# Kernel optimization log

Hardware: AMD Instinct MI355X
Metric: run time of the kernel (lower is better)

## Reference

```python
import jax, jax.numpy as jnp
import numpy as np

SUBSTEP = 10
FRAMES = 24
T = FRAMES * SUBSTEP
DT = 1.0 / 60.0 / SUBSTEP
SLOPE_DEG = 20.0
COS_S = float(np.cos(np.deg2rad(SLOPE_DEG)))
SIN_S = float(np.sin(np.deg2rad(SLOPE_DEG)))
INIT_HEIGHT = 0.1
N_VERTS = 2_000_000
GRAVITY = jnp.array([0.0, -9.8, 0.0], dtype=jnp.float32)
CONTACT_N = jnp.array([-SIN_S, COS_S, 0.0], dtype=jnp.float32)
EPS = 1e-6


def quat_mul(a, b):
    w1, x1, y1, z1 = a[0], a[1], a[2], a[3]
    w2, x2, y2, z2 = b[0], b[1], b[2], b[3]
    return jnp.stack([
        w1 * w2 - x1 * x2 - y1 * y2 - z1 * z2,
        w1 * x2 + x1 * w2 + y1 * z2 - z1 * y2,
        w1 * y2 + y1 * w2 + z1 * x2 - x1 * z2,
        w1 * z2 + z1 * w2 + x1 * y2 - y1 * x2,
    ])


def quat_to_matrix(q):
    q = q / jnp.linalg.norm(q)
    w, x, y, z = q[0], q[1], q[2], q[3]
    return jnp.stack([
        jnp.stack([1 - 2 * y * y - 2 * z * z, 2 * x * y - 2 * w * z, 2 * x * z + 2 * w * y]),
        jnp.stack([2 * x * y + 2 * w * z, 1 - 2 * x * x - 2 * z * z, 2 * y * z - 2 * w * x]),
        jnp.stack([2 * x * z - 2 * w * y, 2 * y * z + 2 * w * x, 1 - 2 * x * x - 2 * y * y]),
    ])


def cross_matrix(a):
    z = jnp.zeros((), dtype=a.dtype)
    return jnp.stack([
        jnp.stack([z, -a[2], a[1]]),
        jnp.stack([a[2], z, -a[0]]),
        jnp.stack([-a[1], a[0], z]),
    ])


def setup_inputs() -> dict:
    key = jax.random.key(0)
    k1, k2, k3 = jax.random.split(key, 3)
    return {
        "x": jax.random.normal(k1, (N_VERTS, 3), dtype=jnp.float32) * 0.2,
        "mass_center": jnp.zeros((3,), dtype=jnp.float32),
        "init_trans": jax.random.normal(k2, (3,), dtype=jnp.float32) * 0.3 + jnp.array([0.3, 0.5, 0.0]),
        "init_quat": jnp.ones((4,), dtype=jnp.float32),
        "init_v": jax.random.normal(k3, (3,), dtype=jnp.float32) * 0.1,
        "kn": jnp.array([0.5], dtype=jnp.float32),
        "mu": jnp.array([0.4], dtype=jnp.float32),
        "linear_damping": jnp.array([0.999], dtype=jnp.float32),
        "angular_damping": jnp.array([0.998], dtype=jnp.float32),
    }


def _simulate(x, mass_center, init_trans, init_quat, init_v, kn, mu, linear_damping, angular_damping):
    n = x.shape[0]
    mass = jnp.asarray(float(n), dtype=x.dtype)  # unit mass per vertex
    inv_mass = 1.0 / mass
    r = x - mass_center
    # inertia_reference = sum_i m*( (r.r) I - outer(r,r) )
    inertia = jnp.sum(jnp.einsum('ni,ni->n', r, r)) * jnp.eye(3, dtype=x.dtype) - jnp.einsum('ni,nj->ij', r, r)
    kn0, mu0 = kn[0], mu[0]
    ld, ad = linear_damping[0], angular_damping[0]
    eye3 = jnp.eye(3, dtype=x.dtype)

    def step(carry, _):
        trans, quat, v, omega = carry
        Rm = quat_to_matrix(quat)
        Rx = x @ Rm.T                                   # [N,3]
        xi = trans + Rx + mass_center                   # world positions
        vi_all = v + jnp.cross(omega[None, :], Rx)      # per-vertex velocities
        d = xi @ CONTACT_N
        rel_v = vi_all @ CONTACT_N
        mask = (d < -COS_S * INIT_HEIGHT) & (rel_v < 0.0)
        num = jnp.sum(mask)
        numf = jnp.maximum(num, 1).astype(x.dtype)
        sum_pos = jnp.sum(x * mask[:, None].astype(x.dtype), axis=0)
        ri = sum_pos / numf
        Ri = Rm @ ri
        vi = v + jnp.cross(omega, Ri)
        v_n = jnp.dot(vi, CONTACT_N) * CONTACT_N
        v_t = vi - v_n
        vn_new = -kn0 * v_n
        alpha = jnp.maximum(1.0 - mu0 * (1.0 + kn0) * (jnp.linalg.norm(v_n) / (jnp.linalg.norm(v_t) + EPS)), 0.0)
        vi_new = vn_new + alpha * v_t
        I = Rm @ inertia @ Rm.T
        I_inv = jnp.linalg.inv(I)
        Rri = cross_matrix(Ri)
        kmat = inv_mass * eye3 - Rri @ I_inv @ Rri
        J = jnp.linalg.solve(kmat, vi_new - vi)
        hit = num > 0
        dv = jnp.where(hit, J * inv_mass, 0.0)
        domega = jnp.where(hit, I_inv @ Rri @ J, 0.0)
        v_new = (v + GRAVITY * DT) * ld + dv
        omega_new = omega * ad + domega
        trans_new = trans + DT * v_new
        wq = jnp.concatenate([jnp.zeros((1,), dtype=x.dtype), omega_new]) * (0.5 * DT)
        quat_new = quat + quat_mul(wq, quat)
        quat_new = quat_new / jnp.linalg.norm(quat_new)
        new_carry = (trans_new, quat_new, v_new, omega_new)
        return new_carry, jnp.concatenate([trans_new, quat_new])

    carry0 = (init_trans, init_quat / jnp.linalg.norm(init_quat), init_v, jnp.zeros(3, dtype=x.dtype))
    _, traj = jax.lax.scan(step, carry0, None, length=T)
    return traj  # [T, 7] = translation(3) + quaternion(4) per substep


def reference(x, mass_center, init_trans, init_quat, init_v, kn, mu, linear_damping, angular_damping):
    return _simulate(x, mass_center, init_trans, init_quat, init_v, kn, mu, linear_damping, angular_damping)
```

## Files before the change

kernel.cpp:

```cpp
#include <hip/hip_runtime.h>

#define GRID   256
#define BLOCK  512
#define NWAVES (BLOCK / 64)
#define CHUNK  7813
#define SLOTS  16
#define NREPT  64

typedef unsigned long long u64;

__device__ __forceinline__ u64 rec_load(const u64* p) {
  return __hip_atomic_load(p, __ATOMIC_RELAXED, __HIP_MEMORY_SCOPE_AGENT);
}
__device__ __forceinline__ void rec_store(u64* p, u64 v) {
  __hip_atomic_store(p, v, __ATOMIC_RELAXED, __HIP_MEMORY_SCOPE_AGENT);
}
__device__ __forceinline__ u64 rec_pack(float f, unsigned tag) {
  return (u64)__float_as_uint(f) | ((u64)tag << 32);
}

#define C_NX   ((float)(-0.3420201433256687))
#define C_NY   ((float)( 0.9396926207859084))
#define C_DTF  ((float)(1.0 / 60.0 / 10.0))
#define C_HDT  ((float)(0.5 * (1.0 / 60.0 / 10.0)))
#define C_DTH  ((float)(-0.9396926207859084 * 0.1))
#define C_GYDT (-9.8f * (float)(1.0 / 60.0 / 10.0))

__device__ __forceinline__ void mat3_mul(const float* A, const float* B, float* C) {
  #pragma unroll
  for (int i = 0; i < 3; ++i)
    #pragma unroll
    for (int j = 0; j < 3; ++j)
      C[i*3+j] = A[i*3+0]*B[0*3+j] + A[i*3+1]*B[1*3+j] + A[i*3+2]*B[2*3+j];
// ... 8 lines not shown
__device__ __forceinline__ void mat3_inv(const float* m, float* inv) {
  float A =  (m[4]*m[8] - m[5]*m[7]);
  float B = -(m[3]*m[8] - m[5]*m[6]);
  float C =  (m[3]*m[7] - m[4]*m[6]);
  float det = m[0]*A + m[1]*B + m[2]*C;
  float id = 1.0f / det;
  inv[0] = A * id;
  inv[1] = -(m[1]*m[8] - m[2]*m[7]) * id;
  inv[2] =  (m[1]*m[5] - m[2]*m[4]) * id;
  inv[3] = B * id;
  inv[4] =  (m[0]*m[8] - m[2]*m[6]) * id;
  inv[5] = -(m[0]*m[5] - m[2]*m[3]) * id;
  inv[6] = C * id;
  inv[7] = -(m[0]*m[7] - m[1]*m[6]) * id;
  inv[8] =  (m[0]*m[4] - m[1]*m[3]) * id;
}

__global__ __launch_bounds__(BLOCK, 2)
void sim_kernel(const float* __restrict__ xg,
                const float* __restrict__ mc_p,
                const float* __restrict__ itr_p,
                const float* __restrict__ iq_p,
                const float* __restrict__ iv_p,
                const float* __restrict__ kn_p,
                const float* __restrict__ mu_p,
                const float* __restrict__ ldp_p,
                const float* __restrict__ adp_p,
                float* __restrict__ out,
                u64* __restrict__ ws,
                int N, int T)
{
  const int tid  = threadIdx.x;
  const int bid  = blockIdx.x;
  const int lane = tid & 63;
  const int wid  = tid >> 6;

  __shared__ float s_redI[NWAVES * 6];
  __shared__ float s_red[2][NWAVES * 4];
  __shared__ float s_gat[NWAVES * 4];

  u64* part = ws;
  u64* tot  = ws + 2 * 4 * GRID;
  u64* bufI = ws + 2 * 4 * GRID + 2 * NREPT * 4;

  const float mc0 = mc_p[0], mc1 = mc_p[1], mc2 = mc_p[2];

  const int vstart = bid * CHUNK;
  int cl = N - vstart; if (cl > CHUNK) cl = CHUNK; if (cl < 0) cl = 0;

  const float NANF = __int_as_float(0x7fc00000);
  float xr0[SLOTS], xr1[SLOTS], xr2[SLOTS];
  #pragma unroll
  for (int s = 0; s < SLOTS; ++s) {
    const int i = tid + s * BLOCK;
    if (i < cl) {
      const float* p = xg + (size_t)(vstart + i) * 3;
      xr0[s] = p[0]; xr1[s] = p[1]; xr2[s] = p[2];
    } else {
      xr0[s] = NANF; xr1[s] = NANF; xr2[s] = NANF;
    }
  }

  {
    float v6[6] = {0,0,0,0,0,0};
    #pragma unroll
    for (int s = 0; s < SLOTS; ++s) {
      if (tid + s * BLOCK < cl) {
        float r0 = xr0[s] - mc0, r1 = xr1[s] - mc1, r2 = xr2[s] - mc2;
        v6[0] += r0*r0; v6[1] += r1*r1; v6[2] += r2*r2;
        v6[3] += r0*r1; v6[4] += r0*r2; v6[5] += r1*r2;
      }
    }
    #pragma unroll
    for (int off = 32; off > 0; off >>= 1)
      #pragma unroll
      for (int k = 0; k < 6; ++k) v6[k] += __shfl_down(v6[k], off, 64);
    if (lane == 0) {
      #pragma unroll
      for (int k = 0; k < 6; ++k) s_redI[wid * 6 + k] = v6[k];
    }
    __syncthreads();
    if (tid == 0) {
      float t6[6];
      #pragma unroll
      for (int k = 0; k < 6; ++k) {
        t6[k] = s_redI[k];
        #pragma unroll
        for (int w = 1; w < NWAVES; ++w) t6[k] += s_redI[w * 6 + k];
      }
      #pragma unroll
      for (int k = 0; k < 6; ++k) rec_store(bufI + k * GRID + bid, rec_pack(t6[k], 0xC0FFEEu));
    }
    __syncthreads();
  }

  float In[9];
  {
    float g6[6] = {0,0,0,0,0,0};
    if (tid < GRID) {
      u64 r[6];
      int f = 0;
      for (;;) {
        #pragma unroll
        for (int k = 0; k < 6; ++k) r[k] = rec_load(bufI + k * GRID + tid);
        bool ok = true;
        #pragma unroll
        for (int k = 0; k < 6; ++k) ok &= ((unsigned)(r[k] >> 32) == 0xC0FFEEu);
        if (ok) break;
        if ((++f & 15) == 0) __builtin_amdgcn_s_sleep(1);
      }
      #pragma unroll
      for (int k = 0; k < 6; ++k) g6[k] = __uint_as_float((unsigned)r[k]);
    }
    #pragma unroll
    for (int off = 32; off > 0; off >>= 1)
      #pragma unroll
      for (int k = 0; k < 6; ++k) g6[k] += __shfl_down(g6[k], off, 64);
    if (lane == 0) {
      #pragma unroll
      for (int k = 0; k < 6; ++k) s_redI[wid * 6 + k] = g6[k];
    }
    __syncthreads();
    float t6[6];
    #pragma unroll
    for (int k = 0; k < 6; ++k) {
      t6[k] = s_redI[k];
      #pragma unroll
      for (int w = 1; w < NWAVES; ++w) t6[k] += s_redI[w * 6 + k];
    }
    float trc = t6[0] + t6[1] + t6[2];
    In[0] = trc - t6[0]; In[4] = trc - t6[1]; In[8] = trc - t6[2];
    In[1] = -t6[3]; In[3] = -t6[3];
    In[2] = -t6[4]; In[6] = -t6[4];
    In[5] = -t6[5]; In[7] = -t6[5];
  }

  float tr0 = itr_p[0], tr1 = itr_p[1], tr2 = itr_p[2];
  float q0 = iq_p[0], q1 = iq_p[1], q2 = iq_p[2], q3 = iq_p[3];
  {
    float n0 = sqrtf(q0*q0 + q1*q1 + q2*q2 + q3*q3);
    q0 /= n0; q1 /= n0; q2 /= n0; q3 /= n0;
  }
  float v0 = iv_p[0], v1 = iv_p[1], v2 = iv_p[2];
  float om0 = 0.f, om1 = 0.f, om2 = 0.f;
  const float knv = kn_p[0], muv = mu_p[0], ldv = ldp_p[0], adv = adp_p[0];
  const float inv_mass = 1.0f / (float)N;

  float Rm[9], Ii[9];
  float pa0, pa1, pa2, pb0, pb1, pb2, pca, pcb;
  int skip;

  {
    float qn = sqrtf(q0*q0 + q1*q1 + q2*q2 + q3*q3);
    float w = q0/qn, xq = q1/qn, yq = q2/qn, zq = q3/qn;
    Rm[0] = 1.f - 2.f*yq*yq - 2.f*zq*zq; Rm[1] = 2.f*xq*yq - 2.f*w*zq; Rm[2] = 2.f*xq*zq + 2.f*w*yq;
    Rm[3] = 2.f*xq*yq + 2.f*w*zq; Rm[4] = 1.f - 2.f*xq*xq - 2.f*zq*zq; Rm[5] = 2.f*yq*zq - 2.f*w*xq;
    Rm[6] = 2.f*xq*zq - 2.f*w*yq; Rm[7] = 2.f*yq*zq + 2.f*w*xq; Rm[8] = 1.f - 2.f*xq*xq - 2.f*yq*yq;
    pa0 = Rm[0]*C_NX + Rm[3]*C_NY;
    pa1 = Rm[1]*C_NX + Rm[4]*C_NY;
    pa2 = Rm[2]*C_NX + Rm[5]*C_NY;
    float w0 = C_NY*om2, w1 = -C_NX*om2, w2 = C_NX*om1 - C_NY*om0;
    pb0 = Rm[0]*w0 + Rm[3]*w1 + Rm[6]*w2;
    pb1 = Rm[1]*w0 + Rm[4]*w1 + Rm[7]*w2;
    pb2 = Rm[2]*w0 + Rm[5]*w1 + Rm[8]*w2;
    pca = C_DTH - ((tr0 + mc0)*C_NX + (tr1 + mc1)*C_NY);
    pcb = -(v0*C_NX + v1*C_NY);
    skip = (om0 == 0.f && om1 == 0.f && om2 == 0.f && !(pcb > 0.f)) ? 1 : 0;
    float Tm[9]; mat3_mul(Rm, In, Tm);
    float Iw[9]; mat3_mul_bt(Tm, Rm, Iw);
    mat3_inv(Iw, Ii);
  }

  int pub = 0;
  for (int t = 0; t < T; ++t) {
    float tn = 0.f, tx = 0.f, ty = 0.f, tz = 0.f;

    if (!skip) {
      const int p = pub & 1;
      const unsigned want = (unsigned)(pub + 1);

      float acc0 = 0.f, acc1 = 0.f, acc2 = 0.f, acc3 = 0.f;
      #pragma unroll
      for (int s = 0; s < SLOTS; ++s) {
        const float x0 = xr0[s], x1 = xr1[s], x2 = xr2[s];
        const float da = x0*pa0 + x1*pa1 + x2*pa2;
        const float db = x0*pb0 + x1*pb1 + x2*pb2;
        if (da < pca && db < pcb) {
          acc0 += 1.f; acc1 += x0; acc2 += x1; acc3 += x2;
        }
      }
      #pragma unroll
      for (int off = 32; off > 0; off >>= 1) {
        acc0 += __shfl_down(acc0, off, 64);
        acc1 += __shfl_down(acc1, off, 64);
        acc2 += __shfl_down(acc2, off, 64);
        acc3 += __shfl_down(acc3, off, 64);
      }
      float* srA = s_red[p];
      if (lane == 0) {
        srA[wid*4+0] = acc0; srA[wid*4+1] = acc1;
        srA[wid*4+2] = acc2; srA[wid*4+3] = acc3;
      }
      __syncthreads();
      if (tid < 4) {
        float tw = srA[tid];
        #pragma unroll
        for (int w2 = 1; w2 < NWAVES; ++w2) tw += srA[w2*4 + tid];
        rec_store(part + (size_t)p * 4 * GRID + (size_t)tid * GRID + bid,
                  rec_pack(tw, want));
      }

      {
        float Tm[9]; mat3_mul(Rm, In, Tm);
        float Iw[9]; mat3_mul_bt(Tm, Rm, Iw);
        mat3_inv(Iw, Ii);
      }

      if (bid == 0) {
        float f0 = 0.f, f1 = 0.f, f2 = 0.f, f3 = 0.f;
        if (tid < GRID) {
          const u64* pp = part + (size_t)p * 4 * GRID + tid;
          u64 r0, r1, r2, r3;
          int fl = 0;
          for (;;) {
            r0 = rec_load(pp + 0 * GRID);
            r1 = rec_load(pp + 1 * GRID);
            r2 = rec_load(pp + 2 * GRID);
            r3 = rec_load(pp + 3 * GRID);
            if (((unsigned)(r0 >> 32) == want) && ((unsigned)(r1 >> 32) == want) &&
                ((unsigned)(r2 >> 32) == want) && ((unsigned)(r3 >> 32) == want)) break;
            if ((++fl & 15) == 0) __builtin_amdgcn_s_sleep(1);
          }
          f0 = __uint_as_float((unsigned)r0);
          f1 = __uint_as_float((unsigned)r1);
          f2 = __uint_as_float((unsigned)r2);
          f3 = __uint_as_float((unsigned)r3);
        }
        #pragma unroll
        for (int off = 32; off > 0; off >>= 1) {
          f0 += __shfl_down(f0, off, 64);
          f1 += __shfl_down(f1, off, 64);
          f2 += __shfl_down(f2, off, 64);
          f3 += __shfl_down(f3, off, 64);
        }
        if (lane == 0) {
          s_gat[wid*4+0] = f0; s_gat[wid*4+1] = f1;
          s_gat[wid*4+2] = f2; s_gat[wid*4+3] = f3;
        }
        __syncthreads();
        tn = s_gat[0]; tx = s_gat[1]; ty = s_gat[2]; tz = s_gat[3];
        #pragma unroll
        for (int w2 = 1; w2 < NWAVES; ++w2) {
          tn += s_gat[w2*4+0]; tx += s_gat[w2*4+1];
          ty += s_gat[w2*4+2]; tz += s_gat[w2*4+3];
        }
        if (tid < NREPT * 4) {
          const int w2 = tid & 3;
          const float val = (w2 == 0) ? tn : (w2 == 1) ? tx : (w2 == 2) ? ty : tz;
          rec_store(tot + (size_t)p * NREPT * 4 + tid, rec_pack(val, want));
        }
      } else {
        const u64* tp = tot + (size_t)p * NREPT * 4 + (size_t)(bid & (NREPT - 1)) * 4;
        u64 r0, r1, r2, r3;
        int fl = 0;
        for (;;) {
          r0 = rec_load(tp + 0); r1 = rec_load(tp + 1);
          r2 = rec_load(tp + 2); r3 = rec_load(tp + 3);
          if (((unsigned)(r0 >> 32) == want) && ((unsigned)(r1 >> 32) == want) &&
              ((unsigned)(r2 >> 32) == want) && ((unsigned)(r3 >> 32) == want)) break;
          if ((++fl & 31) == 0) __builtin_amdgcn_s_sleep(1);
        }
        tn = __uint_as_float((unsigned)r0);
        tx = __uint_as_float((unsigned)r1);
        ty = __uint_as_float((unsigned)r2);
        tz = __uint_as_float((unsigned)r3);
      }
      ++pub;
    }

    {
      float dv0 = 0.f, dv1 = 0.f, dv2 = 0.f, dm0 = 0.f, dm1 = 0.f, dm2 = 0.f;
      if (tn > 0.0f) {
        float numf = fmaxf(tn, 1.0f);
        float ri0 = tx/numf, ri1 = ty/numf, ri2 = tz/numf;
        float Ri0 = Rm[0]*ri0 + Rm[1]*ri1 + Rm[2]*ri2;
        float Ri1 = Rm[3]*ri0 + Rm[4]*ri1 + Rm[5]*ri2;
        float Ri2 = Rm[6]*ri0 + Rm[7]*ri1 + Rm[8]*ri2;
        float vi0 = v0 + om1*Ri2 - om2*Ri1;
        float vi1 = v1 + om2*Ri0 - om0*Ri2;
        float vi2 = v2 + om0*Ri1 - om1*Ri0;
        float vdn = vi0*C_NX + vi1*C_NY;
        float vn0 = vdn*C_NX, vn1 = vdn*C_NY;
        float vt0 = vi0 - vn0, vt1 = vi1 - vn1, vt2 = vi2;
        float nvn = sqrtf(vn0*vn0 + vn1*vn1);
        float nvt = sqrtf(vt0*vt0 + vt1*vt1 + vt2*vt2);
        float alpha = fmaxf(1.0f - muv*(1.0f + knv)*(nvn/(nvt + 1e-6f)), 0.0f);
        float dvi0 = (-knv*vn0 + alpha*vt0) - vi0;
        float dvi1 = (-knv*vn1 + alpha*vt1) - vi1;
        float dvi2 = (alpha*vt2) - vi2;
        float Cx[9] = {0.f, -Ri2, Ri1,  Ri2, 0.f, -Ri0,  -Ri1, Ri0, 0.f};
        float T2[9]; mat3_mul(Cx, Ii, T2);
        float T3[9]; mat3_mul(T2, Cx, T3);
        float Km[9];
        #pragma unroll
        for (int m = 0; m < 9; ++m) Km[m] = -T3[m];
        Km[0] += inv_mass; Km[4] += inv_mass; Km[8] += inv_mass;
        float Ki[9]; mat3_inv(Km, Ki);
        float J0 = Ki[0]*dvi0 + Ki[1]*dvi1 + Ki[2]*dvi2;
        float J1 = Ki[3]*dvi0 + Ki[4]*dvi1 + Ki[5]*dvi2;
        float J2 = Ki[6]*dvi0 + Ki[7]*dvi1 + Ki[8]*dvi2;
        dv0 = J0*inv_mass; dv1 = J1*inv_mass; dv2 = J2*inv_mass;
        float c0 = -Ri2*J1 + Ri1*J2;
        float c1 =  Ri2*J0 - Ri0*J2;
        float c2 = -Ri1*J0 + Ri0*J1;
        dm0 = Ii[0]*c0 + Ii[1]*c1 + Ii[2]*c2;
        dm1 = Ii[3]*c0 + Ii[4]*c1 + Ii[5]*c2;
        dm2 = Ii[6]*c0 + Ii[7]*c1 + Ii[8]*c2;
      }
      v0 = v0*ldv + dv0;
      v1 = (v1 + C_GYDT)*ldv + dv1;
      v2 = v2*ldv + dv2;
      om0 = om0*adv + dm0; om1 = om1*adv + dm1; om2 = om2*adv + dm2;
      tr0 += C_DTF*v0; tr1 += C_DTF*v1; tr2 += C_DTF*v2;
      float wx = om0*C_HDT, wy = om1*C_HDT, wz = om2*C_HDT;
      float dq0 = -wx*q1 - wy*q2 - wz*q3;
      float dq1 =  wx*q0 + wy*q3 - wz*q2;
      float dq2 =  wy*q0 + wz*q1 - wx*q3;
      float dq3 =  wz*q0 + wx*q2 - wy*q1;
      q0 += dq0; q1 += dq1; q2 += dq2; q3 += dq3;
      float qn2 = sqrtf(q0*q0 + q1*q1 + q2*q2 + q3*q3);
      q0 /= qn2; q1 /= qn2; q2 /= qn2; q3 /= qn2;
      if (bid == 0 && tid == 0) {
        float* o = out + (size_t)t * 7;
        o[0] = tr0; o[1] = tr1; o[2] = tr2;
        o[3] = q0;  o[4] = q1;  o[5] = q2;  o[6] = q3;
      }
      float qn = sqrtf(q0*q0 + q1*q1 + q2*q2 + q3*q3);
      float w = q0/qn, xq = q1/qn, yq = q2/qn, zq = q3/qn;
      Rm[0] = 1.f - 2.f*yq*yq - 2.f*zq*zq; Rm[1] = 2.f*xq*yq - 2.f*w*zq; Rm[2] = 2.f*xq*zq + 2.f*w*yq;
      Rm[3] = 2.f*xq*yq + 2.f*w*zq; Rm[4] = 1.f - 2.f*xq*xq - 2.f*zq*zq; Rm[5] = 2.f*yq*zq - 2.f*w*xq;
      Rm[6] = 2.f*xq*zq - 2.f*w*yq; Rm[7] = 2.f*yq*zq + 2.f*w*xq; Rm[8] = 1.f - 2.f*xq*xq - 2.f*yq*yq;
      pa0 = Rm[0]*C_NX + Rm[3]*C_NY;
      pa1 = Rm[1]*C_NX + Rm[4]*C_NY;
      pa2 = Rm[2]*C_NX + Rm[5]*C_NY;
      float w0 = C_NY*om2, w1 = -C_NX*om2, w2 = C_NX*om1 - C_NY*om0;
      pb0 = Rm[0]*w0 + Rm[3]*w1 + Rm[6]*w2;
      pb1 = Rm[1]*w0 + Rm[4]*w1 + Rm[7]*w2;
      pb2 = Rm[2]*w0 + Rm[5]*w1 + Rm[8]*w2;
      pca = C_DTH - ((tr0 + mc0)*C_NX + (tr1 + mc1)*C_NY);
      pcb = -(v0*C_NX + v1*C_NY);
      skip = (om0 == 0.f && om1 == 0.f && om2 == 0.f && !(pcb > 0.f)) ? 1 : 0;
    }
  }
}

extern "C" void kernel_launch(void* const* d_in, const int* in_sizes, int n_in,
                              void* d_out, int out_size, void* d_ws, size_t ws_size,
                              hipStream_t stream) {
  const float* x   = (const float*)d_in[0];
  const float* mc  = (const float*)d_in[1];
  const float* itr = (const float*)d_in[2];
  const float* iq  = (const float*)d_in[3];
  const float* iv  = (const float*)d_in[4];
  const float* kn  = (const float*)d_in[5];
  const float* mu  = (const float*)d_in[6];
  const float* ldp = (const float*)d_in[7];
  const float* adp = (const float*)d_in[8];
  float* out = (float*)d_out;
  u64* ws  = (u64*)d_ws;
  int N = in_sizes[0] / 3;
  int T = out_size / 7;

  void* args[] = {(void*)&x, (void*)&mc, (void*)&itr, (void*)&iq, (void*)&iv,
                  (void*)&kn, (void*)&mu, (void*)&ldp, (void*)&adp,
                  (void*)&out, (void*)&ws, (void*)&N, (void*)&T};
  hipLaunchCooperativeKernel((void*)sim_kernel, dim3(GRID), dim3(BLOCK),
                             args, 0, stream);
}
```

Baseline: 1.430 ms.

## Gather near-plane candidate vertices to leader block and iterate locally

Moves the per-step simulation onto block 0, which drives the other blocks through a request/mode protocol. Worker blocks scan their register-resident vertices against a widened plane threshold and publish the few near-contact candidates into a workspace buffer. The leader caches these candidates in LDS and runs several substeps on them alone, using a bound built from the maximum vertex radius to decide when to re-scan or fall back to a full grid reduction. This replaces the per-step grid-wide reduction and synchronisation with occasional scans, at the cost of a leader-serialised loop and correctness that depends on the conservative bound and the candidate capacity overflow path.

```diff
diff --git a/kernel.cpp b/kernel.cpp
--- a/kernel.cpp
+++ b/kernel.cpp
@@ -1,13 +1,23 @@
 #include <hip/hip_runtime.h>
 
-#define GRID   256
-#define BLOCK  512
-#define NWAVES (BLOCK / 64)
-#define CHUNK  7813
-#define SLOTS  16
-#define NREPT  64
+#define GRID    256
+#define BLOCK   512
+#define NWAVES  (BLOCK / 64)
+#define CHUNK   7813
+#define SLOTS   16
+#define NREPR   64
+#define CAP     96
+#define CSTRIDE 296
+#define CAPTOT  4096
+#define EPSB    0.03f
+
+#define MODE_SCAN 1u
+#define MODE_FULL 2u
+#define MODE_DONE 3u
 
 typedef unsigned long long u64;
+typedef unsigned int u32;
+
 
 __device__ __forceinline__ u64 rec_load(const u64* p) {
   return __hip_atomic_load(p, __ATOMIC_RELAXED, __HIP_MEMORY_SCOPE_AGENT);
@@ -17,6 +27,9 @@
 }
 __device__ __forceinline__ u64 rec_pack(float f, unsigned tag) {
   return (u64)__float_as_uint(f) | ((u64)tag << 32);
+}
+__device__ __forceinline__ u64 rec_pack_u(u32 v, unsigned tag) {
+  return (u64)v | ((u64)tag << 32);
 }
 
 #define C_NX   ((float)(-0.3420201433256687))
@@ -55,6 +68,167 @@
   inv[6] = C * id;
   inv[7] = -(m[0]*m[7] - m[1]*m[6]) * id;
   inv[8] =  (m[0]*m[4] - m[1]*m[3]) * id;
+}
+
+__device__ __forceinline__ void scan_publish(
+    const float* xr0, const float* xr1, const float* xr2,
+    float A0, float A1, float A2, float THR,
+    unsigned rrnd, u64* region, u32* s_wc )
+{
+  const int tid = threadIdx.x, lane = tid & 63, wid = tid >> 6;
+  #pragma unroll
+  for (int s = 0; s < SLOTS; ++s) {
+    float da = xr0[s]*A0 + xr1[s]*A1 + xr2[s]*A2;
+    u64 m = __ballot(da < THR);
+    if (lane == 0) s_wc[s*NWAVES + wid] = (u32)__popcll(m);
+  }
+  __syncthreads();
+  int runbase = 0;
+  #pragma unroll
+  for (int s = 0; s < SLOTS; ++s) {
+    int wb = 0, tot = 0;
+    #pragma unroll
+    for (int w = 0; w < NWAVES; ++w) {
+      u32 c = s_wc[s*NWAVES + w];
+      if (w < wid) wb += (int)c;
+      tot += (int)c;
+    }
+    const float x0 = xr0[s], x1 = xr1[s], x2 = xr2[s];
+    const float da = x0*A0 + x1*A1 + x2*A2;
+    const bool pred = (da < THR);
+    const u64 m = __ballot(pred);
+    if (pred) {
+      int pos = runbase + wb + (int)__popcll(m & ((1ull << lane) - 1ull));
+      if (pos < CAP) {
+        u64* dp = region + 1 + 3*(size_t)pos;
+        rec_store(dp + 0, rec_pack(x0, rrnd));
+        rec_store(dp + 1, rec_pack(x1, rrnd));
+        rec_store(dp + 2, rec_pack(x2, rrnd));
+      }
+    }
+    runbase += tot;
+  }
+  if (tid == 0) rec_store(region, rec_pack_u((u32)runbase, rrnd));
+  __syncthreads();
+}
+
+__device__ __forceinline__ void full_publish(
+    const float* xr0, const float* xr1, const float* xr2,
+    float A0, float A1, float A2, float CAv,
+    float B0, float B1, float B2, float CBv,
+    unsigned rrnd, u64* part, int bid, float* s_red)
+{
+  const int tid = threadIdx.x, lane = tid & 63, wid = tid >> 6;
+  float a0 = 0.f, a1 = 0.f, a2 = 0.f, a3 = 0.f;
+  #pragma unroll
+  for (int s = 0; s < SLOTS; ++s) {
+    const float x0 = xr0[s], x1 = xr1[s], x2 = xr2[s];
+    const float da = x0*A0 + x1*A1 + x2*A2;
+    const float db = x0*B0 + x1*B1 + x2*B2;
+    if (da < CAv && db < CBv) { a0 += 1.f; a1 += x0; a2 += x1; a3 += x2; }
+  }
+  #pragma unroll
+  for (int off = 32; off > 0; off >>= 1) {
+    a0 += __shfl_down(a0, off, 64);
+    a1 += __shfl_down(a1, off, 64);
+    a2 += __shfl_down(a2, off, 64);
+    a3 += __shfl_down(a3, off, 64);
+  }
+  if (lane == 0) {
+    s_red[wid*4+0] = a0; s_red[wid*4+1] = a1;
+    s_red[wid*4+2] = a2; s_red[wid*4+3] = a3;
+  }
+  __syncthreads();
+  if (tid < 4) {
+    float tw = s_red[tid];
+    #pragma unroll
+    for (int w = 1; w < NWAVES; ++w) tw += s_red[w*4 + tid];
+    rec_store(part + (size_t)tid * GRID + bid, rec_pack(tw, rrnd));
+  }
+  __syncthreads();
+}
+
+__device__ __forceinline__ void leader_step(
+    float tn, float tx, float ty, float tz,
+    float& tr0, float& tr1, float& tr2,
+    float& q0, float& q1, float& q2, float& q3,
+    float& v0, float& v1, float& v2,
+    float& om0, float& om1, float& om2,
+    float (&Rm)[9], const float (&In)[9],
+    float knv, float muv, float ldv, float adv, float inv_mass,
+    float mc0, float mc1,
+    float* s_plane, float* outp)
+{
+  float dv0 = 0.f, dv1 = 0.f, dv2 = 0.f, dm0 = 0.f, dm1 = 0.f, dm2 = 0.f;
+  if (tn > 0.0f) {
+    float Tm[9]; mat3_mul(Rm, In, Tm);
+    float Iw[9]; mat3_mul_bt(Tm, Rm, Iw);
+    float Ii[9]; mat3_inv(Iw, Ii);
+    float numf = fmaxf(tn, 1.0f);
+    float ri0 = tx/numf, ri1 = ty/numf, ri2 = tz/numf;
+    float Ri0 = Rm[0]*ri0 + Rm[1]*ri1 + Rm[2]*ri2;
+    float Ri1 = Rm[3]*ri0 + Rm[4]*ri1 + Rm[5]*ri2;
+    float Ri2 = Rm[6]*ri0 + Rm[7]*ri1 + Rm[8]*ri2;
+    float vi0 = v0 + om1*Ri2 - om2*Ri1;
+    float vi1 = v1 + om2*Ri0 - om0*Ri2;
+    float vi2 = v2 + om0*Ri1 - om1*Ri0;
+    float vdn = vi0*C_NX + vi1*C_NY;
+    float vn0 = vdn*C_NX, vn1 = vdn*C_NY;
+    float vt0 = vi0 - vn0, vt1 = vi1 - vn1, vt2 = vi2;
+    float nvn = sqrtf(vn0*vn0 + vn1*vn1);
+    float nvt = sqrtf(vt0*vt0 + vt1*vt1 + vt2*vt2);
+    float alpha = fmaxf(1.0f - muv*(1.0f + knv)*(nvn/(nvt + 1e-6f)), 0.0f);
+    float dvi0 = (-knv*vn0 + alpha*vt0) - vi0;
+    float dvi1 = (-knv*vn1 + alpha*vt1) - vi1;
+    float dvi2 = (alpha*vt2) - vi2;
+    float Cx[9] = {0.f, -Ri2, Ri1,  Ri2, 0.f, -Ri0,  -Ri1, Ri0, 0.f};
+    float T2[9]; mat3_mul(Cx, Ii, T2);
+    float T3[9]; mat3_mul(T2, Cx, T3);
+    float Km[9];
+    #pragma unroll
+    for (int m = 0; m < 9; ++m) Km[m] = -T3[m];
+    Km[0] += inv_mass; Km[4] += inv_mass; Km[8] += inv_mass;
+    float Ki[9]; mat3_inv(Km, Ki);
+    float J0 = Ki[0]*dvi0 + Ki[1]*dvi1 + Ki[2]*dvi2;
+    float J1 = Ki[3]*dvi0 + Ki[4]*dvi1 + Ki[5]*dvi2;
+    float J2 = Ki[6]*dvi0 + Ki[7]*dvi1 + Ki[8]*dvi2;
+    dv0 = J0*inv_mass; dv1 = J1*inv_mass; dv2 = J2*inv_mass;
+    float c0 = -Ri2*J1 + Ri1*J2;
+    float c1 =  Ri2*J0 - Ri0*J2;
+    float c2 = -Ri1*J0 + Ri0*J1;
+    dm0 = Ii[0]*c0 + Ii[1]*c1 + Ii[2]*c2;
+    dm1 = Ii[3]*c0 + Ii[4]*c1 + Ii[5]*c2;
+    dm2 = Ii[6]*c0 + Ii[7]*c1 + Ii[8]*c2;
+  }
+  v0 = v0*ldv + dv0;
+  v1 = (v1 + C_GYDT)*ldv + dv1;
+  v2 = v2*ldv + dv2;
+  om0 = om0*adv + dm0; om1 = om1*adv + dm1; om2 = om2*adv + dm2;
+  tr0 += C_DTF*v0; tr1 += C_DTF*v1; tr2 += C_DTF*v2;
+  float wx = om0*C_HDT, wy = om1*C_HDT, wz = om2*C_HDT;
+  float dq0 = -wx*q1 - wy*q2 - wz*q3;
+  float dq1 =  wx*q0 + wy*q3 - wz*q2;
+  float dq2 =  wy*q0 + wz*q1 - wx*q3;
+  float dq3 =  wz*q0 + wx*q2 - wy*q1;
+  q0 += dq0; q1 += dq1; q2 += dq2; q3 += dq3;
+  float qn2 = sqrtf(q0*q0 + q1*q1 + q2*q2 + q3*q3);
+  q0 /= qn2; q1 /= qn2; q2 /= qn2; q3 /= qn2;
+  outp[0] = tr0; outp[1] = tr1; outp[2] = tr2;
+  outp[3] = q0;  outp[4] = q1;  outp[5] = q2;  outp[6] = q3;
+  float qn = sqrtf(q0*q0 + q1*q1 + q2*q2 + q3*q3);
+  float w = q0/qn, xq = q1/qn, yq = q2/qn, zq = q3/qn;
+  Rm[0] = 1.f - 2.f*yq*yq - 2.f*zq*zq; Rm[1] = 2.f*xq*yq - 2.f*w*zq; Rm[2] = 2.f*xq*zq + 2.f*w*yq;
+  Rm[3] = 2.f*xq*yq + 2.f*w*zq; Rm[4] = 1.f - 2.f*xq*xq - 2.f*zq*zq; Rm[5] = 2.f*yq*zq - 2.f*w*xq;
+  Rm[6] = 2.f*xq*zq - 2.f*w*yq; Rm[7] = 2.f*yq*zq + 2.f*w*xq; Rm[8] = 1.f - 2.f*xq*xq - 2.f*yq*yq;
+  s_plane[0] = Rm[0]*C_NX + Rm[3]*C_NY;
+  s_plane[1] = Rm[1]*C_NX + Rm[4]*C_NY;
+  s_plane[2] = Rm[2]*C_NX + Rm[5]*C_NY;
+  float w0 = C_NY*om2, w1 = -C_NX*om2, w2 = C_NX*om1 - C_NY*om0;
+  s_plane[4] = Rm[0]*w0 + Rm[3]*w1 + Rm[6]*w2;
+  s_plane[5] = Rm[1]*w0 + Rm[4]*w1 + Rm[7]*w2;
+  s_plane[6] = Rm[2]*w0 + Rm[5]*w1 + Rm[8]*w2;
+  s_plane[3] = C_DTH - ((tr0 + mc0)*C_NX + (tr1 + mc1)*C_NY);
+  s_plane[7] = -(v0*C_NX + v1*C_NY);
 }
 
 __global__ __launch_bounds__(BLOCK, 2)
@@ -76,13 +250,25 @@
   const int lane = tid & 63;
   const int wid  = tid >> 6;
 
-  __shared__ float s_redI[NWAVES * 6];
-  __shared__ float s_red[2][NWAVES * 4];
-  __shared__ float s_gat[NWAVES * 4];
-
-  u64* part = ws;
-  u64* tot  = ws + 2 * 4 * GRID;
-  u64* bufI = ws + 2 * 4 * GRID + 2 * NREPT * 4;
+  __shared__ float s_redI[NWAVES * 7];
+  __shared__ float s_red[NWAVES * 4];
+  __shared__ float s_plane[8];
+  __shared__ u32   s_reqw[16];
+  __shared__ u32   s_cnt[GRID];
+  __shared__ u32   s_wc[SLOTS * NWAVES];
+  __shared__ u32   s_act;
+  __shared__ u32   s_total;
+
+  extern __shared__ float dyn[];
+  float* cx = dyn;
+  float* cy = dyn + CAPTOT;
+  float* cz = dyn + 2 * CAPTOT;
+  u32*   cmap = (u32*)(dyn + 3 * CAPTOT);
+
+  u64* req  = ws;
+  u64* part = ws + 1024;
+  u64* bufI = ws + 2048;
+  u64* cand = ws + 3840;
 
   const float mc0 = mc_p[0], mc1 = mc_p[1], mc2 = mc_p[2];
 
@@ -103,294 +289,344 @@
   }
 
   {
-    float v6[6] = {0,0,0,0,0,0};
+    float v7[7] = {0,0,0,0,0,0,0};
     #pragma unroll
     for (int s = 0; s < SLOTS; ++s) {
       if (tid + s * BLOCK < cl) {
         float r0 = xr0[s] - mc0, r1 = xr1[s] - mc1, r2 = xr2[s] - mc2;
-        v6[0] += r0*r0; v6[1] += r1*r1; v6[2] += r2*r2;
-        v6[3] += r0*r1; v6[4] += r0*r2; v6[5] += r1*r2;
-      }
-    }
-    #pragma unroll
-    for (int off = 32; off > 0; off >>= 1)
-      #pragma unroll
-      for (int k = 0; k < 6; ++k) v6[k] += __shfl_down(v6[k], off, 64);
+        v7[0] += r0*r0; v7[1] += r1*r1; v7[2] += r2*r2;
+        v7[3] += r0*r1; v7[4] += r0*r2; v7[5] += r1*r2;
+        float n2 = xr0[s]*xr0[s] + xr1[s]*xr1[s] + xr2[s]*xr2[s];
+        v7[6] = fmaxf(v7[6], n2);
+      }
+    }
+    #pragma unroll
+    for (int off = 32; off > 0; off >>= 1) {
+      #pragma unroll
+      for (int k = 0; k < 6; ++k) v7[k] += __shfl_down(v7[k], off, 64);
+      v7[6] = fmaxf(v7[6], __shfl_down(v7[6], off, 64));
+    }
     if (lane == 0) {
       #pragma unroll
-      for (int k = 0; k < 6; ++k) s_redI[wid * 6 + k] = v6[k];
+      for (int k = 0; k < 7; ++k) s_redI[wid * 7 + k] = v7[k];
     }
     __syncthreads();
     if (tid == 0) {
-      float t6[6];
-      #pragma unroll
-      for (int k = 0; k < 6; ++k) {
-        t6[k] = s_redI[k];
+      float t7[7];
+      #pragma unroll
+      for (int k = 0; k < 7; ++k) t7[k] = s_redI[k];
+      #pragma unroll
+      for (int w = 1; w < NWAVES; ++w) {
         #pragma unroll
-        for (int w = 1; w < NWAVES; ++w) t6[k] += s_redI[w * 6 + k];
-      }
-      #pragma unroll
-      for (int k = 0; k < 6; ++k) rec_store(bufI + k * GRID + bid, rec_pack(t6[k], 0xC0FFEEu));
+        for (int k = 0; k < 6; ++k) t7[k] += s_redI[w * 7 + k];
+        t7[6] = fmaxf(t7[6], s_redI[w * 7 + 6]);
+      }
+      #pragma unroll
+      for (int k = 0; k < 7; ++k)
+        rec_store(bufI + (size_t)k * GRID + bid, rec_pack(t7[k], 0xC0FFEEu));
     }
     __syncthreads();
   }
 
+  if (bid != 0) {
+    unsigned rrnd = 1;
+    for (;;) {
+      if (tid < 16) {
+        const u64* rl = req + (size_t)(bid & (NREPR - 1)) * 16 + tid;
+        u64 r; int f = 0;
+        for (;;) {
+          r = rec_load(rl);
+          if ((unsigned)(r >> 32) == rrnd) break;
+          if ((++f & 31) == 0) __builtin_amdgcn_s_sleep(4);
+        }
+        s_reqw[tid] = (u32)r;
+      }
+      __syncthreads();
+      const u32 mode = s_reqw[9];
+      if (mode == MODE_DONE) return;
+      const float A0 = __uint_as_float(s_reqw[0]);
+      const float A1 = __uint_as_float(s_reqw[1]);
+      const float A2 = __uint_as_float(s_reqw[2]);
+      if (mode == MODE_SCAN) {
+        const float THR = __uint_as_float(s_reqw[8]);
+        scan_publish(xr0, xr1, xr2, A0, A1, A2, THR, rrnd,
+                     cand + (size_t)bid * CSTRIDE, s_wc);
+      } else {
+        const float CAv = __uint_as_float(s_reqw[3]);
+        const float B0 = __uint_as_float(s_reqw[4]);
+        const float B1 = __uint_as_float(s_reqw[5]);
+        const float B2 = __uint_as_float(s_reqw[6]);
+        const float CBv = __uint_as_float(s_reqw[7]);
+        full_publish(xr0, xr1, xr2, A0, A1, A2, CAv, B0, B1, B2, CBv,
+                     rrnd, part, bid, s_red);
+      }
+      ++rrnd;
+      __syncthreads();
+    }
+  }
+
   float In[9];
+  float maxX = 0.f;
   {
-    float g6[6] = {0,0,0,0,0,0};
+    float g7[7] = {0,0,0,0,0,0,0};
     if (tid < GRID) {
-      u64 r[6];
-      int f = 0;
+      u64 r[7]; int f = 0;
       for (;;) {
         #pragma unroll
-        for (int k = 0; k < 6; ++k) r[k] = rec_load(bufI + k * GRID + tid);
+        for (int k = 0; k < 7; ++k) r[k] = rec_load(bufI + (size_t)k * GRID + tid);
         bool ok = true;
         #pragma unroll
-        for (int k = 0; k < 6; ++k) ok &= ((unsigned)(r[k] >> 32) == 0xC0FFEEu);
+        for (int k = 0; k < 7; ++k) ok &= ((unsigned)(r[k] >> 32) == 0xC0FFEEu);
         if (ok) break;
         if ((++f & 15) == 0) __builtin_amdgcn_s_sleep(1);
       }
       #pragma unroll
-      for (int k = 0; k < 6; ++k) g6[k] = __uint_as_float((unsigned)r[k]);
-    }
-    #pragma unroll
-    for (int off = 32; off > 0; off >>= 1)
-      #pragma unroll
-      for (int k = 0; k < 6; ++k) g6[k] += __shfl_down(g6[k], off, 64);
+      for (int k = 0; k < 7; ++k) g7[k] = __uint_as_float((unsigned)r[k]);
+    }
+    #pragma unroll
+    for (int off = 32; off > 0; off >>= 1) {
+      #pragma unroll
+      for (int k = 0; k < 6; ++k) g7[k] += __shfl_down(g7[k], off, 64);
+      g7[6] = fmaxf(g7[6], __shfl_down(g7[6], off, 64));
+    }
     if (lane == 0) {
       #pragma unroll
-      for (int k = 0; k < 6; ++k) s_redI[wid * 6 + k] = g6[k];
+      for (int k = 0; k < 7; ++k) s_redI[wid * 7 + k] = g7[k];
     }
     __syncthreads();
-    float t6[6];
-    #pragma unroll
-    for (int k = 0; k < 6; ++k) {
-      t6[k] = s_redI[k];
-      #pragma unroll
-      for (int w = 1; w < NWAVES; ++w) t6[k] += s_redI[w * 6 + k];
-    }
-    float trc = t6[0] + t6[1] + t6[2];
-    In[0] = trc - t6[0]; In[4] = trc - t6[1]; In[8] = trc - t6[2];
-    In[1] = -t6[3]; In[3] = -t6[3];
-    In[2] = -t6[4]; In[6] = -t6[4];
-    In[5] = -t6[5]; In[7] = -t6[5];
-  }
-
-  float tr0 = itr_p[0], tr1 = itr_p[1], tr2 = itr_p[2];
-  float q0 = iq_p[0], q1 = iq_p[1], q2 = iq_p[2], q3 = iq_p[3];
-  {
+    float t7[7];
+    #pragma unroll
+    for (int k = 0; k < 7; ++k) t7[k] = s_redI[k];
+    #pragma unroll
+    for (int w = 1; w < NWAVES; ++w) {
+      #pragma unroll
+      for (int k = 0; k < 6; ++k) t7[k] += s_redI[w * 7 + k];
+      t7[6] = fmaxf(t7[6], s_redI[w * 7 + 6]);
+    }
+    float trc = t7[0] + t7[1] + t7[2];
+    In[0] = trc - t7[0]; In[4] = trc - t7[1]; In[8] = trc - t7[2];
+    In[1] = -t7[3]; In[3] = -t7[3];
+    In[2] = -t7[4]; In[6] = -t7[4];
+    In[5] = -t7[5]; In[7] = -t7[5];
+    maxX = sqrtf(t7[6]);
+  }
+
+  float tr0, tr1, tr2, q0, q1, q2, q3, v0, v1, v2, om0, om1, om2;
+  float Rm[9];
+  const float knv = kn_p[0], muv = mu_p[0], ldv = ldp_p[0], adv = adp_p[0];
+  const float inv_mass = 1.0f / (float)N;
+  if (tid == 0) {
+    tr0 = itr_p[0]; tr1 = itr_p[1]; tr2 = itr_p[2];
+    q0 = iq_p[0]; q1 = iq_p[1]; q2 = iq_p[2]; q3 = iq_p[3];
     float n0 = sqrtf(q0*q0 + q1*q1 + q2*q2 + q3*q3);
     q0 /= n0; q1 /= n0; q2 /= n0; q3 /= n0;
-  }
-  float v0 = iv_p[0], v1 = iv_p[1], v2 = iv_p[2];
-  float om0 = 0.f, om1 = 0.f, om2 = 0.f;
-  const float knv = kn_p[0], muv = mu_p[0], ldv = ldp_p[0], adv = adp_p[0];
-  const float inv_mass = 1.0f / (float)N;
-
-  float Rm[9], Ii[9];
-  float pa0, pa1, pa2, pb0, pb1, pb2, pca, pcb;
-  int skip;
-
-  {
+    v0 = iv_p[0]; v1 = iv_p[1]; v2 = iv_p[2];
+    om0 = 0.f; om1 = 0.f; om2 = 0.f;
     float qn = sqrtf(q0*q0 + q1*q1 + q2*q2 + q3*q3);
     float w = q0/qn, xq = q1/qn, yq = q2/qn, zq = q3/qn;
     Rm[0] = 1.f - 2.f*yq*yq - 2.f*zq*zq; Rm[1] = 2.f*xq*yq - 2.f*w*zq; Rm[2] = 2.f*xq*zq + 2.f*w*yq;
     Rm[3] = 2.f*xq*yq + 2.f*w*zq; Rm[4] = 1.f - 2.f*xq*xq - 2.f*zq*zq; Rm[5] = 2.f*yq*zq - 2.f*w*xq;
     Rm[6] = 2.f*xq*zq - 2.f*w*yq; Rm[7] = 2.f*yq*zq + 2.f*w*xq; Rm[8] = 1.f - 2.f*xq*xq - 2.f*yq*yq;
-    pa0 = Rm[0]*C_NX + Rm[3]*C_NY;
-    pa1 = Rm[1]*C_NX + Rm[4]*C_NY;
-    pa2 = Rm[2]*C_NX + Rm[5]*C_NY;
+    s_plane[0] = Rm[0]*C_NX + Rm[3]*C_NY;
+    s_plane[1] = Rm[1]*C_NX + Rm[4]*C_NY;
+    s_plane[2] = Rm[2]*C_NX + Rm[5]*C_NY;
     float w0 = C_NY*om2, w1 = -C_NX*om2, w2 = C_NX*om1 - C_NY*om0;
-    pb0 = Rm[0]*w0 + Rm[3]*w1 + Rm[6]*w2;
-    pb1 = Rm[1]*w0 + Rm[4]*w1 + Rm[7]*w2;
-    pb2 = Rm[2]*w0 + Rm[5]*w1 + Rm[8]*w2;
-    pca = C_DTH - ((tr0 + mc0)*C_NX + (tr1 + mc1)*C_NY);
-    pcb = -(v0*C_NX + v1*C_NY);
-    skip = (om0 == 0.f && om1 == 0.f && om2 == 0.f && !(pcb > 0.f)) ? 1 : 0;
-    float Tm[9]; mat3_mul(Rm, In, Tm);
-    float Iw[9]; mat3_mul_bt(Tm, Rm, Iw);
-    mat3_inv(Iw, Ii);
-  }
-
-  int pub = 0;
-  for (int t = 0; t < T; ++t) {
-    float tn = 0.f, tx = 0.f, ty = 0.f, tz = 0.f;
-
-    if (!skip) {
-      const int p = pub & 1;
-      const unsigned want = (unsigned)(pub + 1);
-
-      float acc0 = 0.f, acc1 = 0.f, acc2 = 0.f, acc3 = 0.f;
-      #pragma unroll
-      for (int s = 0; s < SLOTS; ++s) {
-        const float x0 = xr0[s], x1 = xr1[s], x2 = xr2[s];
-        const float da = x0*pa0 + x1*pa1 + x2*pa2;
-        const float db = x0*pb0 + x1*pb1 + x2*pb2;
-        if (da < pca && db < pcb) {
-          acc0 += 1.f; acc1 += x0; acc2 += x1; acc3 += x2;
+    s_plane[4] = Rm[0]*w0 + Rm[3]*w1 + Rm[6]*w2;
+    s_plane[5] = Rm[1]*w0 + Rm[4]*w1 + Rm[7]*w2;
+    s_plane[6] = Rm[2]*w0 + Rm[5]*w1 + Rm[8]*w2;
+    s_plane[3] = C_DTH - ((tr0 + mc0)*C_NX + (tr1 + mc1)*C_NY);
+    s_plane[7] = -(v0*C_NX + v1*C_NY);
+  }
+  __syncthreads();
+
+  unsigned rrnd = 1;
+  int t = 0;
+  int fullsteps = 0;
+  float ar0, ar1, ar2, thr_r;
+
+  for (;;) {
+    if (t >= T) {
+      if (tid == 0) { s_reqw[9] = MODE_DONE; }
+      __syncthreads();
+      for (int i = tid; i < NREPR * 16; i += BLOCK) {
+        u32 pay = ((i & 15) == 9) ? MODE_DONE : 0u;
+        rec_store(req + i, rec_pack_u(pay, rrnd));
+      }
+      return;
+    }
+
+    if (fullsteps > 0) {
+      if (tid == 0) {
+        #pragma unroll
+        for (int k = 0; k < 8; ++k) s_reqw[k] = __float_as_uint(s_plane[k] * 1.0f);
+        s_reqw[8] = 0u; s_reqw[9] = MODE_FULL;
+        #pragma unroll
+        for (int k = 10; k < 16; ++k) s_reqw[k] = 0u;
+      }
+      __syncthreads();
+      for (int i = tid; i < NREPR * 16; i += BLOCK)
+        rec_store(req + i, rec_pack_u(s_reqw[i & 15], rrnd));
+      full_publish(xr0, xr1, xr2,
+                   s_plane[0], s_plane[1], s_plane[2], s_plane[3],
+                   s_plane[4], s_plane[5], s_plane[6], s_plane[7],
+                   rrnd, part, 0, s_red);
+      float f0 = 0.f, f1 = 0.f, f2 = 0.f, f3 = 0.f;
+      if (tid < GRID) {
+        const u64* pp = part + tid;
+        u64 r0, r1, r2, r3; int fl = 0;
+        for (;;) {
+          r0 = rec_load(pp + 0 * GRID);
+          r1 = rec_load(pp + 1 * GRID);
+          r2 = rec_load(pp + 2 * GRID);
+          r3 = rec_load(pp + 3 * GRID);
+          if (((unsigned)(r0 >> 32) == rrnd) && ((unsigned)(r1 >> 32) == rrnd) &&
+              ((unsigned)(r2 >> 32) == rrnd) && ((unsigned)(r3 >> 32) == rrnd)) break;
+          if ((++fl & 15) == 0) __builtin_amdgcn_s_sleep(1);
         }
+        f0 = __uint_as_float((unsigned)r0);
+        f1 = __uint_as_float((unsigned)r1);
+        f2 = __uint_as_float((unsigned)r2);
+        f3 = __uint_as_float((unsigned)r3);
       }
       #pragma unroll
       for (int off = 32; off > 0; off >>= 1) {
-        acc0 += __shfl_down(acc0, off, 64);
-        acc1 += __shfl_down(acc1, off, 64);
-        acc2 += __shfl_down(acc2, off, 64);
-        acc3 += __shfl_down(acc3, off, 64);
-      }
-      float* srA = s_red[p];
+        f0 += __shfl_down(f0, off, 64);
+        f1 += __shfl_down(f1, off, 64);
+        f2 += __shfl_down(f2, off, 64);
+        f3 += __shfl_down(f3, off, 64);
+      }
       if (lane == 0) {
-        srA[wid*4+0] = acc0; srA[wid*4+1] = acc1;
-        srA[wid*4+2] = acc2; srA[wid*4+3] = acc3;
-      }
-      __syncthreads();
-      if (tid < 4) {
-        float tw = srA[tid];
+        s_red[wid*4+0] = f0; s_red[wid*4+1] = f1;
+        s_red[wid*4+2] = f2; s_red[wid*4+3] = f3;
+      }
+      __syncthreads();
+      if (tid == 0) {
+        float tn = s_red[0], tx = s_red[1], ty = s_red[2], tz = s_red[3];
         #pragma unroll
-        for (int w2 = 1; w2 < NWAVES; ++w2) tw += srA[w2*4 + tid];
-        rec_store(part + (size_t)p * 4 * GRID + (size_t)tid * GRID + bid,
-                  rec_pack(tw, want));
-      }
-
-      {
-        float Tm[9]; mat3_mul(Rm, In, Tm);
-        float Iw[9]; mat3_mul_bt(Tm, Rm, Iw);
-        mat3_inv(Iw, Ii);
-      }
-
-      if (bid == 0) {
-        float f0 = 0.f, f1 = 0.f, f2 = 0.f, f3 = 0.f;
-        if (tid < GRID) {
-          const u64* pp = part + (size_t)p * 4 * GRID + tid;
-          u64 r0, r1, r2, r3;
-          int fl = 0;
-          for (;;) {
-            r0 = rec_load(pp + 0 * GRID);
-            r1 = rec_load(pp + 1 * GRID);
-            r2 = rec_load(pp + 2 * GRID);
-            r3 = rec_load(pp + 3 * GRID);
-            if (((unsigned)(r0 >> 32) == want) && ((unsigned)(r1 >> 32) == want) &&
-                ((unsigned)(r2 >> 32) == want) && ((unsigned)(r3 >> 32) == want)) break;
-            if ((++fl & 15) == 0) __builtin_amdgcn_s_sleep(1);
-          }
-          f0 = __uint_as_float((unsigned)r0);
-          f1 = __uint_as_float((unsigned)r1);
-          f2 = __uint_as_float((unsigned)r2);
-          f3 = __uint_as_float((unsigned)r3);
+        for (int w = 1; w < NWAVES; ++w) {
+          tn += s_red[w*4+0]; tx += s_red[w*4+1];
+          ty += s_red[w*4+2]; tz += s_red[w*4+3];
         }
+        leader_step(tn, tx, ty, tz, tr0, tr1, tr2, q0, q1, q2, q3,
+                    v0, v1, v2, om0, om1, om2, Rm, In,
+                    knv, muv, ldv, adv, inv_mass, mc0, mc1,
+                    s_plane, out + (size_t)t * 7);
+      }
+      ++t; ++rrnd; --fullsteps;
+      __syncthreads();
+      continue;
+    }
+
+    if (tid == 0) {
+      s_reqw[0] = __float_as_uint(s_plane[0]);
+      s_reqw[1] = __float_as_uint(s_plane[1]);
+      s_reqw[2] = __float_as_uint(s_plane[2]);
+      s_reqw[3] = __float_as_uint(s_plane[3]);
+      s_reqw[4] = __float_as_uint(s_plane[4]);
+      s_reqw[5] = __float_as_uint(s_plane[5]);
+      s_reqw[6] = __float_as_uint(s_plane[6]);
+      s_reqw[7] = __float_as_uint(s_plane[7]);
+      s_reqw[8] = __float_as_uint(s_plane[3] + EPSB);
+      s_reqw[9] = MODE_SCAN;
+      #pragma unroll
+      for (int k = 10; k < 16; ++k) s_reqw[k] = 0u;
+      ar0 = s_plane[0]; ar1 = s_plane[1]; ar2 = s_plane[2];
+      thr_r = s_plane[3] + EPSB;
+    }
+    __syncthreads();
+    for (int i = tid; i < NREPR * 16; i += BLOCK)
+      rec_store(req + i, rec_pack_u(s_reqw[i & 15], rrnd));
+    scan_publish(xr0, xr1, xr2, s_plane[0], s_plane[1], s_plane[2],
+                 s_plane[3] + EPSB, rrnd, cand, s_wc);
+    if (tid < GRID) {
+      const u64* cp = cand + (size_t)tid * CSTRIDE;
+      u64 r; int f = 0;
+      for (;;) {
+        r = rec_load(cp);
+        if ((unsigned)(r >> 32) == rrnd) break;
+        if ((++f & 15) == 0) __builtin_amdgcn_s_sleep(1);
+      }
+      s_cnt[tid] = (u32)r;
+    }
+    __syncthreads();
+    if (tid == 0) {
+      u32 total = 0, ovf = 0;
+      for (int b = 0; b < GRID; ++b) {
+        u32 c = s_cnt[b];
+        if (c > CAP || total + c > CAPTOT) { ovf = 1; break; }
+        for (u32 j = 0; j < c; ++j) cmap[total++] = ((u32)b << 16) | j;
+      }
+      s_total = total; s_act = ovf;
+    }
+    __syncthreads();
+    if (s_act) {
+      ++rrnd;
+      fullsteps = 4;
+      continue;
+    }
+    {
+      const int tot = (int)s_total;
+      for (int c = tid; c < tot; c += BLOCK) {
+        u32 e = cmap[c];
+        const u64* dp = cand + (size_t)(e >> 16) * CSTRIDE + 1 + 3 * (size_t)(e & 0xFFFFu);
+        u64 w0, w1, w2; int f = 0;
+        for (;;) {
+          w0 = rec_load(dp + 0); w1 = rec_load(dp + 1); w2 = rec_load(dp + 2);
+          if (((unsigned)(w0 >> 32) == rrnd) && ((unsigned)(w1 >> 32) == rrnd) &&
+              ((unsigned)(w2 >> 32) == rrnd)) break;
+          if ((++f & 15) == 0) __builtin_amdgcn_s_sleep(1);
+        }
+        cx[c] = __uint_as_float((unsigned)w0);
+        cy[c] = __uint_as_float((unsigned)w1);
+        cz[c] = __uint_as_float((unsigned)w2);
+      }
+    }
+    ++rrnd;
+    __syncthreads();
+
+    for (;;) {
+      const float A0 = s_plane[0], A1 = s_plane[1], A2 = s_plane[2], CAv = s_plane[3];
+      const float B0 = s_plane[4], B1 = s_plane[5], B2 = s_plane[6], CBv = s_plane[7];
+      float a0 = 0.f, a1 = 0.f, a2 = 0.f, a3 = 0.f;
+      const int tot = (int)s_total;
+      for (int c = tid; c < tot; c += BLOCK) {
+        const float x0 = cx[c], x1 = cy[c], x2 = cz[c];
+        const float da = x0*A0 + x1*A1 + x2*A2;
+        const float db = x0*B0 + x1*B1 + x2*B2;
+        if (da < CAv && db < CBv) { a0 += 1.f; a1 += x0; a2 += x1; a3 += x2; }
+      }
+      #pragma unroll
+      for (int off = 32; off > 0; off >>= 1) {
+        a0 += __shfl_down(a0, off, 64);
+        a1 += __shfl_down(a1, off, 64);
+        a2 += __shfl_down(a2, off, 64);
+        a3 += __shfl_down(a3, off, 64);
+      }
+      if (lane == 0) {
+        s_red[wid*4+0] = a0; s_red[wid*4+1] = a1;
+        s_red[wid*4+2] = a2; s_red[wid*4+3] = a3;
+      }
+      __syncthreads();
+      if (tid == 0) {
+        float tn = s_red[0], tx = s_red[1], ty = s_red[2], tz = s_red[3];
         #pragma unroll
-        for (int off = 32; off > 0; off >>= 1) {
-          f0 += __shfl_down(f0, off, 64);
-          f1 += __shfl_down(f1, off, 64);
-          f2 += __shfl_down(f2, off, 64);
-          f3 += __shfl_down(f3, off, 64);
+        for (int w = 1; w < NWAVES; ++w) {
+          tn += s_red[w*4+0]; tx += s_red[w*4+1];
+          ty += s_red[w*4+2]; tz += s_red[w*4+3];
         }
-        if (lane == 0) {
-          s_gat[wid*4+0] = f0; s_gat[wid*4+1] = f1;
-          s_gat[wid*4+2] = f2; s_gat[wid*4+3] = f3;
-        }
-        __syncthreads();
-        tn = s_gat[0]; tx = s_gat[1]; ty = s_gat[2]; tz = s_gat[3];
-        #pragma unroll
-        for (int w2 = 1; w2 < NWAVES; ++w2) {
-          tn += s_gat[w2*4+0]; tx += s_gat[w2*4+1];
-          ty += s_gat[w2*4+2]; tz += s_gat[w2*4+3];
-        }
-        if (tid < NREPT * 4) {
-          const int w2 = tid & 3;
-          const float val = (w2 == 0) ? tn : (w2 == 1) ? tx : (w2 == 2) ? ty : tz;
-          rec_store(tot + (size_t)p * NREPT * 4 + tid, rec_pack(val, want));
-        }
-      } else {
-        const u64* tp = tot + (size_t)p * NREPT * 4 + (size_t)(bid & (NREPT - 1)) * 4;
-        u64 r0, r1, r2, r3;
-        int fl = 0;
-        for (;;) {
-          r0 = rec_load(tp + 0); r1 = rec_load(tp + 1);
-          r2 = rec_load(tp + 2); r3 = rec_load(tp + 3);
-          if (((unsigned)(r0 >> 32) == want) && ((unsigned)(r1 >> 32) == want) &&
-              ((unsigned)(r2 >> 32) == want) && ((unsigned)(r3 >> 32) == want)) break;
-          if ((++fl & 31) == 0) __builtin_amdgcn_s_sleep(1);
-        }
-        tn = __uint_as_float((unsigned)r0);
-        tx = __uint_as_float((unsigned)r1);
-        ty = __uint_as_float((unsigned)r2);
-        tz = __uint_as_float((unsigned)r3);
-      }
-      ++pub;
-    }
-
-    {
-      float dv0 = 0.f, dv1 = 0.f, dv2 = 0.f, dm0 = 0.f, dm1 = 0.f, dm2 = 0.f;
-      if (tn > 0.0f) {
-        float numf = fmaxf(tn, 1.0f);
-        float ri0 = tx/numf, ri1 = ty/numf, ri2 = tz/numf;
-        float Ri0 = Rm[0]*ri0 + Rm[1]*ri1 + Rm[2]*ri2;
-        float Ri1 = Rm[3]*ri0 + Rm[4]*ri1 + Rm[5]*ri2;
-        float Ri2 = Rm[6]*ri0 + Rm[7]*ri1 + Rm[8]*ri2;
-        float vi0 = v0 + om1*Ri2 - om2*Ri1;
-        float vi1 = v1 + om2*Ri0 - om0*Ri2;
-        float vi2 = v2 + om0*Ri1 - om1*Ri0;
-        float vdn = vi0*C_NX + vi1*C_NY;
-        float vn0 = vdn*C_NX, vn1 = vdn*C_NY;
-        float vt0 = vi0 - vn0, vt1 = vi1 - vn1, vt2 = vi2;
-        float nvn = sqrtf(vn0*vn0 + vn1*vn1);
-        float nvt = sqrtf(vt0*vt0 + vt1*vt1 + vt2*vt2);
-        float alpha = fmaxf(1.0f - muv*(1.0f + knv)*(nvn/(nvt + 1e-6f)), 0.0f);
-        float dvi0 = (-knv*vn0 + alpha*vt0) - vi0;
-        float dvi1 = (-knv*vn1 + alpha*vt1) - vi1;
-        float dvi2 = (alpha*vt2) - vi2;
-        float Cx[9] = {0.f, -Ri2, Ri1,  Ri2, 0.f, -Ri0,  -Ri1, Ri0, 0.f};
-        float T2[9]; mat3_mul(Cx, Ii, T2);
-        float T3[9]; mat3_mul(T2, Cx, T3);
-        float Km[9];
-        #pragma unroll
-        for (int m = 0; m < 9; ++m) Km[m] = -T3[m];
-        Km[0] += inv_mass; Km[4] += inv_mass; Km[8] += inv_mass;
-        float Ki[9]; mat3_inv(Km, Ki);
-        float J0 = Ki[0]*dvi0 + Ki[1]*dvi1 + Ki[2]*dvi2;
-        float J1 = Ki[3]*dvi0 + Ki[4]*dvi1 + Ki[5]*dvi2;
-        float J2 = Ki[6]*dvi0 + Ki[7]*dvi1 + Ki[8]*dvi2;
-        dv0 = J0*inv_mass; dv1 = J1*inv_mass; dv2 = J2*inv_mass;
-        float c0 = -Ri2*J1 + Ri1*J2;
-        float c1 =  Ri2*J0 - Ri0*J2;
-        float c2 = -Ri1*J0 + Ri0*J1;
-        dm0 = Ii[0]*c0 + Ii[1]*c1 + Ii[2]*c2;
-        dm1 = Ii[3]*c0 + Ii[4]*c1 + Ii[5]*c2;
-        dm2 = Ii[6]*c0 + Ii[7]*c1 + Ii[8]*c2;
-      }
-      v0 = v0*ldv + dv0;
-      v1 = (v1 + C_GYDT)*ldv + dv1;
-      v2 = v2*ldv + dv2;
-      om0 = om0*adv + dm0; om1 = om1*adv + dm1; om2 = om2*adv + dm2;
-      tr0 += C_DTF*v0; tr1 += C_DTF*v1; tr2 += C_DTF*v2;
-      float wx = om0*C_HDT, wy = om1*C_HDT, wz = om2*C_HDT;
-      float dq0 = -wx*q1 - wy*q2 - wz*q3;
-      float dq1 =  wx*q0 + wy*q3 - wz*q2;
-      float dq2 =  wy*q0 + wz*q1 - wx*q3;
-      float dq3 =  wz*q0 + wx*q2 - wy*q1;
-      q0 += dq0; q1 += dq1; q2 += dq2; q3 += dq3;
-      float qn2 = sqrtf(q0*q0 + q1*q1 + q2*q2 + q3*q3);
-      q0 /= qn2; q1 /= qn2; q2 /= qn2; q3 /= qn2;
-      if (bid == 0 && tid == 0) {
-        float* o = out + (size_t)t * 7;
-        o[0] = tr0; o[1] = tr1; o[2] = tr2;
-        o[3] = q0;  o[4] = q1;  o[5] = q2;  o[6] = q3;
-      }
-      float qn = sqrtf(q0*q0 + q1*q1 + q2*q2 + q3*q3);
-      float w = q0/qn, xq = q1/qn, yq = q2/qn, zq = q3/qn;
-      Rm[0] = 1.f - 2.f*yq*yq - 2.f*zq*zq; Rm[1] = 2.f*xq*yq - 2.f*w*zq; Rm[2] = 2.f*xq*zq + 2.f*w*yq;
-      Rm[3] = 2.f*xq*yq + 2.f*w*zq; Rm[4] = 1.f - 2.f*xq*xq - 2.f*zq*zq; Rm[5] = 2.f*yq*zq - 2.f*w*xq;
-      Rm[6] = 2.f*xq*zq - 2.f*w*yq; Rm[7] = 2.f*yq*zq + 2.f*w*xq; Rm[8] = 1.f - 2.f*xq*xq - 2.f*yq*yq;
-      pa0 = Rm[0]*C_NX + Rm[3]*C_NY;
-      pa1 = Rm[1]*C_NX + Rm[4]*C_NY;
-      pa2 = Rm[2]*C_NX + Rm[5]*C_NY;
-      float w0 = C_NY*om2, w1 = -C_NX*om2, w2 = C_NX*om1 - C_NY*om0;
-      pb0 = Rm[0]*w0 + Rm[3]*w1 + Rm[6]*w2;
-      pb1 = Rm[1]*w0 + Rm[4]*w1 + Rm[7]*w2;
-      pb2 = Rm[2]*w0 + Rm[5]*w1 + Rm[8]*w2;
-      pca = C_DTH - ((tr0 + mc0)*C_NX + (tr1 + mc1)*C_NY);
-      pcb = -(v0*C_NX + v1*C_NY);
-      skip = (om0 == 0.f && om1 == 0.f && om2 == 0.f && !(pcb > 0.f)) ? 1 : 0;
+        leader_step(tn, tx, ty, tz, tr0, tr1, tr2, q0, q1, q2, q3,
+                    v0, v1, v2, om0, om1, om2, Rm, In,
+                    knv, muv, ldv, adv, inv_mass, mc0, mc1,
+                    s_plane, out + (size_t)t * 7);
+        float d0 = s_plane[0] - ar0, d1 = s_plane[1] - ar1, d2 = s_plane[2] - ar2;
+        float dA = sqrtf(d0*d0 + d1*d1 + d2*d2);
+        int ok = (s_plane[3] + dA * maxX * 1.0001f + 1e-6f <= thr_r) ? 1 : 0;
+        s_act = (t + 1 >= T) ? 2u : (ok ? 0u : 1u);
+      }
+      __syncthreads();
+      ++t;
+      if (s_act == 0u) continue;
+      break;
     }
   }
 }
@@ -412,9 +648,13 @@
   int N = in_sizes[0] / 3;
   int T = out_size / 7;
 
+  const int dyn_lds = 4 * CAPTOT * 4;
+  hipFuncSetAttribute((const void*)sim_kernel,
+                      hipFuncAttributeMaxDynamicSharedMemorySize, dyn_lds);
+
   void* args[] = {(void*)&x, (void*)&mc, (void*)&itr, (void*)&iq, (void*)&iv,
                   (void*)&kn, (void*)&mu, (void*)&ldp, (void*)&adp,
                   (void*)&out, (void*)&ws, (void*)&N, (void*)&T};
   hipLaunchCooperativeKernel((void*)sim_kernel, dim3(GRID), dim3(BLOCK),
-                             args, 0, stream);
-}
+                             args, dyn_lds, stream);
+}
```

After: 1.896 ms. 1.33x slower.
